# Optimization experiments

Hardware: AMD Instinct MI355X
Metric: run time of the kernel (lower is better)

Reference implementation:

```python
import jax, jax.numpy as jnp
import numpy as np

B, S, D, H = 2, 2048, 1024, 16
HD = D // H  # head dim = 64

def setup_inputs() -> dict:
    key = jax.random.key(0)
    k1, k2, k3 = jax.random.split(key, 3)
    return {
        "hidden_state": jax.random.normal(k1, (B, S, D), dtype=jnp.float32),
        "attention_mask": jnp.ones((B, S), dtype=jnp.float32),
        "w_attn": jax.random.normal(k2, (D, 3 * D), dtype=jnp.float32) * 0.02,
        "b_attn": jnp.zeros((3 * D,), dtype=jnp.float32),
        "w_proj": jax.random.normal(k3, (D, D), dtype=jnp.float32) * 0.02,
        "b_proj": jnp.zeros((D,), dtype=jnp.float32),
    }

def reference(hidden_state, attention_mask, w_attn, b_attn, w_proj, b_proj):
    x = hidden_state  # [B,S,D]
    # Conv1D: F.linear(x, weight.T, bias) == x @ weight + bias
    qkv = x @ w_attn + b_attn  # [B,S,3D]
    q, k, v = jnp.split(qkv, 3, axis=-1)
    def heads(t):  # [B,S,D] -> [B,H,S,HD]
        return t.reshape(B, S, H, HD).transpose(0, 2, 1, 3)
    q, k, v = heads(q), heads(k), heads(v)
    # scaled scores
    scores = jnp.einsum("bhqd,bhkd->bhqk", q, k) / jnp.sqrt(jnp.float32(HD))
    # mask: expand (B,S)->(B,S,S) along keys, tril, 1-that, !=0 -> -inf
    m = jnp.broadcast_to(attention_mask[:, None, :], (B, S, S))
    neg = 1.0 - jnp.tril(m)  # nonzero where disallowed
    bias = jnp.where(neg != 0.0, -jnp.inf, 0.0)  # [B,S,S]
    scores = scores + bias[:, None, :, :]
    attn = jax.nn.softmax(scores, axis=-1)  # [B,H,S,S] (dropout p=0)
    ctx = jnp.einsum("bhqk,bhkd->bhqd", attn, v)  # [B,H,S,HD]
    ctx = ctx.transpose(0, 2, 1, 3).reshape(B, S, D)
    out = ctx @ w_proj + b_proj  # resid dropout p=0
    # original returns attention.transpose(0,1): (H,B,S,S)->(B,H,S,S)
    return out, attn
```

## Files before the change

### kernel.cpp

```cpp
#include <hip/hip_runtime.h>

#define S_ 2048
#define D_ 1024
#define H_ 16
#define HD_ 64

typedef __attribute__((ext_vector_type(8))) short short8;
typedef __attribute__((ext_vector_type(4))) float floatx4;

#define MFMA16(a, b, c) __builtin_amdgcn_mfma_f32_16x16x32_bf16(a, b, c, 0, 0, 0)
#define EXP2 __builtin_amdgcn_exp2f

__device__ __forceinline__ unsigned short f2bf(float f) {
    union { float f; unsigned int u; } v; v.f = f;
    unsigned int r = v.u + 0x7FFFu + ((v.u >> 16) & 1u);
    return (unsigned short)(r >> 16);
}

__device__ __forceinline__ void gll16(const unsigned short* g, unsigned short* l) {
    __builtin_amdgcn_global_load_lds(
        (const __attribute__((address_space(1))) void*)g,
        (__attribute__((address_space(3))) void*)l, 16, 0, 0);
}

__global__ __launch_bounds__(256) void cast_bf16(const float* __restrict__ in,
                                                 unsigned short* __restrict__ out, int n4) {
    int i = blockIdx.x * 256 + threadIdx.x;
    if (i < n4) {
        float4 v = ((const float4*)in)[i];
        ushort4 o;
        o.x = f2bf(v.x); o.y = f2bf(v.y); o.z = f2bf(v.z); o.w = f2bf(v.w);
        ((ushort4*)out)[i] = o;
    }
}

__global__ __launch_bounds__(256) void transpose_cast(const float* __restrict__ W,
                                                      unsigned short* __restrict__ WT,
                                                      int K, int N) {
    __shared__ float tb[64][65];
    const int t = threadIdx.x;
    const int tr = t >> 4, tc = t & 15;
    const int n0 = blockIdx.x * 64, k0 = blockIdx.y * 64;
#pragma unroll
    for (int p = 0; p < 4; ++p) {
        const int r = p * 16 + tr;
        const float4 v = *(const float4*)&W[(size_t)(k0 + r) * N + n0 + tc * 4];
        tb[r][tc * 4 + 0] = v.x; tb[r][tc * 4 + 1] = v.y;
        tb[r][tc * 4 + 2] = v.z; tb[r][tc * 4 + 3] = v.w;
    }
    __syncthreads();
#pragma unroll
    for (int p = 0; p < 4; ++p) {
        const int rn = p * 16 + tr;
        ushort4 o;
        o.x = f2bf(tb[tc * 4 + 0][rn]); o.y = f2bf(tb[tc * 4 + 1][rn]);
        o.z = f2bf(tb[tc * 4 + 2][rn]); o.w = f2bf(tb[tc * 4 + 3][rn]);
        *(ushort4*)&WT[(size_t)(n0 + rn) * K + k0 + tc * 4] = o;
    }
}

__global__ __launch_bounds__(256) void gemm_bt(
    const unsigned short* __restrict__ A, const unsigned short* __restrict__ Bt,
    const float* __restrict__ bias, float* __restrict__ outp,
    unsigned short* __restrict__ qw, unsigned short* __restrict__ kw,
    unsigned short* __restrict__ vtw, int M, int N, int K, int mode)
{
    __shared__ unsigned short As[2][128 * 32];
    __shared__ unsigned short Bs[2][128 * 32];

    const int tid = threadIdx.x;
    const int w = tid >> 6, lane = tid & 63;
    const int l15 = lane & 15, qd = lane >> 4;
    const int wr = w >> 1, wc = w & 1;
    const int row0 = blockIdx.y * 128, col0 = blockIdx.x * 128;

    floatx4 acc[4][4];
#pragma unroll
    for (int i = 0; i < 4; ++i)
#pragma unroll
        for (int j = 0; j < 4; ++j) acc[i][j] = (floatx4){0.f, 0.f, 0.f, 0.f};

    const int sr = tid >> 2;
    const int gs = (tid & 3) ^ ((tid >> 3) & 3);
    const unsigned short* Ab0 = A + (size_t)(row0 + sr) * K + gs * 8;
    const unsigned short* Ab1 = A + (size_t)(row0 + 64 + sr) * K + gs * 8;
    const unsigned short* Bb0 = Bt + (size_t)(col0 + sr) * K + gs * 8;
    const unsigned short* Bb1 = Bt + (size_t)(col0 + 64 + sr) * K + gs * 8;

    auto stage = [&](int bi, int k0) {
        gll16(Ab0 + k0, &As[bi][tid * 8]);
        gll16(Ab1 + k0, &As[bi][(256 + tid) * 8]);
        gll16(Bb0 + k0, &Bs[bi][tid * 8]);
        gll16(Bb1 + k0, &Bs[bi][(256 + tid) * 8]);
    };

    stage(0, 0);
    const int nk = K >> 5;
    for (int it = 0; it < nk; ++it) {
        __syncthreads();
        if (it + 1 < nk) stage((it + 1) & 1, (it + 1) << 5);
        const unsigned short* Asb = As[it & 1];
        const unsigned short* Bsb = Bs[it & 1];
        short8 af[4], bfr[4];
#pragma unroll
        for (int mi = 0; mi < 4; ++mi) {
            const int ra = wr * 64 + mi * 16 + l15;
            af[mi] = *(const short8*)&Asb[ra * 32 + ((qd ^ ((ra >> 1) & 3)) << 3)];
        }
#pragma unroll
        for (int ni = 0; ni < 4; ++ni) {
            const int rb = wc * 64 + ni * 16 + l15;
            bfr[ni] = *(const short8*)&Bsb[rb * 32 + ((qd ^ ((rb >> 1) & 3)) << 3)];
        }
#pragma unroll
        for (int mi = 0; mi < 4; ++mi)
#pragma unroll
            for (int ni = 0; ni < 4; ++ni)
                acc[mi][ni] = MFMA16(af[mi], bfr[ni], acc[mi][ni]);
    }

#pragma unroll
    for (int mi = 0; mi < 4; ++mi)
#pragma unroll
        for (int ni = 0; ni < 4; ++ni) {
            const int col = col0 + wc * 64 + ni * 16 + l15;
            const float bv = bias[col];
#pragma unroll
            for (int r = 0; r < 4; ++r) {
                const int row = row0 + wr * 64 + mi * 16 + qd * 4 + r;
                const float v = acc[mi][ni][r] + bv;
                if (mode == 0) {
                    __builtin_nontemporal_store(v, &outp[(size_t)row * N + col]);
                } else {
                    const int region = col >> 10;
                    const int hh = (col >> 6) & 15;
                    const int dd = col & 63;
                    const int bb = row >> 11;
                    const int ss = row & 2047;
                    const unsigned short bvv = f2bf(v);
                    if (region == 0)
                        qw[((size_t)(bb * 16 + hh) * 2048 + ss) * 64 + dd] = bvv;
                    else if (region == 1)
                        kw[((size_t)(bb * 16 + hh) * 2048 + ss) * 64 + dd] = bvv;
                    else
                        vtw[((size_t)(bb * 16 + hh) * 64 + dd) * 2048 + ss] = bvv;
                }
            }
        }
}

__global__ __launch_bounds__(256) void attn_mfma(
    const unsigned short* __restrict__ qg, const unsigned short* __restrict__ kg,
    const unsigned short* __restrict__ vtg, const float* __restrict__ mask,
    float* __restrict__ attnOut, unsigned short* __restrict__ ctxOut)
{
    __shared__ unsigned short Qb[64 * 64];
    __shared__ unsigned short Kb[2][64 * 64];
    __shared__ unsigned short Vb[2][64 * 64];
    __shared__ unsigned short Ps[64 * 80];
    __shared__ float maskS[2][64];

    const int tid = threadIdx.x;
    const int w = tid >> 6, lane = tid & 63;
    const int l15 = lane & 15, qd = lane >> 4;
    const int x = blockIdx.x;
    const int bh = x & 31;
    const int qt = 31 - (x >> 5);
    const int b = bh >> 4, h = bh & 15;
    const size_t base = (size_t)bh * (S_ * HD_);
    const float SC = 0.18033688f;

    const int sr = tid >> 3;
    const int sp = tid & 7;
    const int gsw = sp ^ (sr & 7);

    auto stageK = [&](int bi, int jt) {
        const unsigned short* gk = kg + base + (size_t)jt * 4096;
        gll16(gk + sr * 64 + gsw * 8, &Kb[bi][tid * 8]);
        gll16(gk + (sr + 32) * 64 + gsw * 8, &Kb[bi][(256 + tid) * 8]);
    };
    auto stageV = [&](int bi, int jt) {
        const unsigned short* gv = vtg + base + jt * 64;
        gll16(gv + (size_t)sr * S_ + gsw * 8, &Vb[bi][tid * 8]);
        gll16(gv + (size_t)(sr + 32) * S_ + gsw * 8, &Vb[bi][(256 + tid) * 8]);
    };

    {
        const unsigned short* gq = qg + base + (size_t)qt * 4096;
        gll16(gq + sr * 64 + gsw * 8, &Qb[tid * 8]);
        gll16(gq + (sr + 32) * 64 + gsw * 8, &Qb[(256 + tid) * 8]);
    }
    stageK(0, 0);
    if (tid < 64) maskS[0][tid] = mask[b * S_ + tid];
    __syncthreads();

    const int qr = w * 16 + l15;
    const short8 aq0 = *(const short8*)&Qb[qr * 64 + ((qd ^ (qr & 7)) << 3)];
    const short8 aq1 = *(const short8*)&Qb[qr * 64 + (((4 + qd) ^ (qr & 7)) << 3)];

    const int qrow_base = qt * 64 + w * 16 + qd * 4;
    float m_i[4], l_i[4], rl[4];
#pragma unroll
    for (int r = 0; r < 4; ++r) { m_i[r] = -3e38f; l_i[r] = 0.f; }

    for (int jt = 0; jt <= qt; ++jt) {
        const int cb = jt & 1;
        if (jt < qt) {
            stageK(cb ^ 1, jt + 1);
            if (tid < 64) maskS[cb ^ 1][tid] = mask[b * S_ + (jt + 1) * 64 + tid];
        }
        float sv[4][4];
        bool mok[4];
        __builtin_amdgcn_s_setprio(1);
#pragma unroll
        for (int ni = 0; ni < 4; ++ni) {
            const int kr = ni * 16 + l15;
            const short8 bk0 = *(const short8*)&Kb[cb][kr * 64 + ((qd ^ (kr & 7)) << 3)];
            const short8 bk1 = *(const short8*)&Kb[cb][kr * 64 + (((4 + qd) ^ (kr & 7)) << 3)];
            floatx4 s = {0.f, 0.f, 0.f, 0.f};
            s = MFMA16(aq0, bk0, s);
            s = MFMA16(aq1, bk1, s);
#pragma unroll
            for (int r = 0; r < 4; ++r) sv[ni][r] = s[r] * SC;
            mok[ni] = (maskS[cb][kr] == 1.0f);
        }
        __builtin_amdgcn_s_setprio(0);
        const bool diag = (jt == qt);
#pragma unroll
        for (int r = 0; r < 4; ++r) {
            const int qrow = qrow_base + r;
            float svr[4], tm = -3e38f;
#pragma unroll
            for (int ni = 0; ni < 4; ++ni) {
                const bool ok = mok[ni] && (!diag || (jt * 64 + ni * 16 + l15 <= qrow));
                svr[ni] = ok ? sv[ni][r] : -3e38f;
                tm = fmaxf(tm, svr[ni]);
            }
            if (tm > -1e37f) {
                const float mn = fmaxf(m_i[r], tm);
                const float sum = EXP2(svr[0] - mn) + EXP2(svr[1] - mn) +
                                  EXP2(svr[2] - mn) + EXP2(svr[3] - mn);
                l_i[r] = l_i[r] * EXP2(m_i[r] - mn) + sum;
                m_i[r] = mn;
            }
        }
        __syncthreads();
    }

#pragma unroll
    for (int r = 0; r < 4; ++r) {
        float m = m_i[r], l = l_i[r];
#pragma unroll
        for (int off = 1; off < 16; off <<= 1) {
            const float mo = __shfl_xor(m, off);
            const float lo = __shfl_xor(l, off);
            const float mn = fmaxf(m, mo);
            l = l * EXP2(m - mn) + lo * EXP2(mo - mn);
            m = mn;
        }
        m_i[r] = m;
        rl[r] = 1.0f / l;
    }

    stageK(0, 0);
    stageV(0, 0);
    if (tid < 64) maskS[0][tid] = mask[b * S_ + tid];

    floatx4 ctxa[4];
#pragma unroll
    for (int ni = 0; ni < 4; ++ni) ctxa[ni] = (floatx4){0.f, 0.f, 0.f, 0.f};
    float* attnBH = attnOut + (size_t)bh * S_ * S_;

    for (int jt = 0; jt < 32; ++jt) {
        if (jt <= qt) {
            const int cb = jt & 1;
            __syncthreads();
            if (jt < qt) {
                stageK(cb ^ 1, jt + 1);
                stageV(cb ^ 1, jt + 1);
                if (tid < 64) maskS[cb ^ 1][tid] = mask[b * S_ + (jt + 1) * 64 + tid];
            }
            float pm[4][4];
            bool mok[4];
            __builtin_amdgcn_s_setprio(1);
#pragma unroll
            for (int ni = 0; ni < 4; ++ni) {
                const int kr = ni * 16 + l15;
                const short8 bk0 = *(const short8*)&Kb[cb][kr * 64 + ((qd ^ (kr & 7)) << 3)];
                const short8 bk1 = *(const short8*)&Kb[cb][kr * 64 + (((4 + qd) ^ (kr & 7)) << 3)];
                floatx4 s = {0.f, 0.f, 0.f, 0.f};
                s = MFMA16(aq0, bk0, s);
                s = MFMA16(aq1, bk1, s);
#pragma unroll
                for (int r = 0; r < 4; ++r) pm[ni][r] = s[r] * SC;
                mok[ni] = (maskS[cb][kr] == 1.0f);
            }
            __builtin_amdgcn_s_setprio(0);
            const bool diag = (jt == qt);
#pragma unroll
            for (int ni = 0; ni < 4; ++ni)
#pragma unroll
                for (int r = 0; r < 4; ++r) {
                    const int qrow = qrow_base + r;
                    const bool ok = mok[ni] && (!diag || (jt * 64 + ni * 16 + l15 <= qrow));
                    const float p = ok ? EXP2(pm[ni][r] - m_i[r]) * rl[r] : 0.0f;
                    pm[ni][r] = p;
                    Ps[(w * 16 + qd * 4 + r) * 80 + ni * 16 + l15] = f2bf(p);
                }
            __syncthreads();
#pragma unroll
            for (int ni = 0; ni < 4; ++ni)
#pragma unroll
                for (int r = 0; r < 4; ++r)
                    __builtin_nontemporal_store(
                        pm[ni][r],
                        &attnBH[(size_t)(qrow_base + r) * S_ + jt * 64 + ni * 16 + l15]);
            __builtin_amdgcn_s_setprio(1);
#pragma unroll
            for (int kk = 0; kk < 2; ++kk) {
                const short8 ap = *(const short8*)&Ps[(w * 16 + l15) * 80 + kk * 32 + qd * 8];
#pragma unroll
                for (int ni = 0; ni < 4; ++ni) {
                    const int vr = ni * 16 + l15;
                    const short8 bv = *(const short8*)
                        &Vb[cb][vr * 64 + (((kk * 4 + qd) ^ (vr & 7)) << 3)];
                    ctxa[ni] = MFMA16(ap, bv, ctxa[ni]);
                }
            }
            __builtin_amdgcn_s_setprio(0);
        } else {
            const floatx4 z = {0.f, 0.f, 0.f, 0.f};
#pragma unroll
            for (int p = 0; p < 4; ++p) {
                const int c = p * 256 + tid;
                const int row = c >> 4, part = c & 15;
                __builtin_nontemporal_store(
                    z, (floatx4*)&attnBH[(size_t)(qt * 64 + row) * S_ + jt * 64 + part * 4]);
            }
        }
    }

#pragma unroll
    for (int ni = 0; ni < 4; ++ni)
#pragma unroll
        for (int r = 0; r < 4; ++r) {
            const int qrow = qrow_base + r;
            ctxOut[((size_t)(b * S_ + qrow)) * D_ + h * 64 + ni * 16 + l15] =
                f2bf(ctxa[ni][r]);
        }
}

extern "C" void kernel_launch(void* const* d_in, const int* in_sizes, int n_in,
                              void* d_out, int out_size, void* d_ws, size_t ws_size,
                              hipStream_t stream) {
    const float* hidden = (const float*)d_in[0];
    const float* mask   = (const float*)d_in[1];
    const float* w_attn = (const float*)d_in[2];
    const float* b_attn = (const float*)d_in[3];
    const float* w_proj = (const float*)d_in[4];
    const float* b_proj = (const float*)d_in[5];

    float* out = (float*)d_out;
    float* attnOut = out + (size_t)2 * S_ * D_;

    unsigned short* ws = (unsigned short*)d_ws;
    const size_t E = (size_t)2 * S_ * D_;
    unsigned short* Xb   = ws;
    unsigned short* WaT  = Xb + E;
    unsigned short* WpT  = WaT + (size_t)3 * D_ * D_;
    unsigned short* qw   = WpT + (size_t)D_ * D_;
    unsigned short* kw   = qw + E;
    unsigned short* vtw  = kw + E;
    unsigned short* ctxb = vtw + E;

    dim3 blk(256);
    cast_bf16<<<dim3((int)(E / 4 / 256)), blk, 0, stream>>>(hidden, Xb, (int)(E / 4));
    transpose_cast<<<dim3(3 * D_ / 64, D_ / 64), blk, 0, stream>>>(w_attn, WaT, D_, 3 * D_);
    transpose_cast<<<dim3(D_ / 64, D_ / 64), blk, 0, stream>>>(w_proj, WpT, D_, D_);

    gemm_bt<<<dim3(3 * D_ / 128, 2 * S_ / 128), blk, 0, stream>>>(
        Xb, WaT, b_attn, nullptr, qw, kw, vtw, 2 * S_, 3 * D_, D_, 1);

    attn_mfma<<<dim3(2 * H_ * (S_ / 64)), blk, 0, stream>>>(
        qw, kw, vtw, mask, attnOut, ctxb);

    gemm_bt<<<dim3(D_ / 128, 2 * S_ / 128), blk, 0, stream>>>(
        ctxb, WpT, b_proj, out, nullptr, nullptr, nullptr, 2 * S_, D_, D_, 0);
}
```

Before: 740.3 us.

## Load K/V/Q directly from global memory and drop block-level LDS staging and barriers

Removes the double-buffered LDS staging of Q, K, V and mask, so each wave reads its MFMA operands straight from global memory (relying on L1/L2 caching) and the P tile goes into a per-wave LDS slice. This eliminates all __syncthreads barriers and lets waves run independently. In exchange, every wave re-reads the same K/V tiles from global memory with uncoalesced 16-byte per-lane loads, and no prefetching overlaps load latency. The Ps write followed by the read within a wave has no explicit wave barrier and relies on wave-synchronous execution.

After: 811.6 us. 1.1x slower.

```diff
diff --git a/kernel.cpp b/kernel.cpp
--- a/kernel.cpp
+++ b/kernel.cpp
@@ -154,11 +154,7 @@
     const unsigned short* __restrict__ vtg, const float* __restrict__ mask,
     float* __restrict__ attnOut, unsigned short* __restrict__ ctxOut)
 {
-    __shared__ unsigned short Qb[64 * 64];
-    __shared__ unsigned short Kb[2][64 * 64];
-    __shared__ unsigned short Vb[2][64 * 64];
-    __shared__ unsigned short Ps[64 * 80];
-    __shared__ float maskS[2][64];
+    __shared__ unsigned short Ps[4][16 * 80];
 
     const int tid = threadIdx.x;
     const int w = tid >> 6, lane = tid & 63;
@@ -170,33 +166,14 @@
     const size_t base = (size_t)bh * (S_ * HD_);
     const float SC = 0.18033688f;
 
-    const int sr = tid >> 3;
-    const int sp = tid & 7;
-    const int gsw = sp ^ (sr & 7);
-
-    auto stageK = [&](int bi, int jt) {
-        const unsigned short* gk = kg + base + (size_t)jt * 4096;
-        gll16(gk + sr * 64 + gsw * 8, &Kb[bi][tid * 8]);
-        gll16(gk + (sr + 32) * 64 + gsw * 8, &Kb[bi][(256 + tid) * 8]);
-    };
-    auto stageV = [&](int bi, int jt) {
-        const unsigned short* gv = vtg + base + jt * 64;
-        gll16(gv + (size_t)sr * S_ + gsw * 8, &Vb[bi][tid * 8]);
-        gll16(gv + (size_t)(sr + 32) * S_ + gsw * 8, &Vb[bi][(256 + tid) * 8]);
-    };
-
-    {
-        const unsigned short* gq = qg + base + (size_t)qt * 4096;
-        gll16(gq + sr * 64 + gsw * 8, &Qb[tid * 8]);
-        gll16(gq + (sr + 32) * 64 + gsw * 8, &Qb[(256 + tid) * 8]);
-    }
-    stageK(0, 0);
-    if (tid < 64) maskS[0][tid] = mask[b * S_ + tid];
-    __syncthreads();
-
-    const int qr = w * 16 + l15;
-    const short8 aq0 = *(const short8*)&Qb[qr * 64 + ((qd ^ (qr & 7)) << 3)];
-    const short8 aq1 = *(const short8*)&Qb[qr * 64 + (((4 + qd) ^ (qr & 7)) << 3)];
+    const unsigned short* Kbh = kg + base;
+    const unsigned short* Vbh = vtg + base;
+    const float* maskB = mask + b * S_;
+    unsigned short* Psw = &Ps[w][0];
+
+    const int qr = qt * 64 + w * 16 + l15;
+    const short8 aq0 = *(const short8*)&qg[base + (size_t)qr * 64 + qd * 8];
+    const short8 aq1 = *(const short8*)&qg[base + (size_t)qr * 64 + 32 + qd * 8];
 
     const int qrow_base = qt * 64 + w * 16 + qd * 4;
     float m_i[4], l_i[4], rl[4];
@@ -204,25 +181,21 @@
     for (int r = 0; r < 4; ++r) { m_i[r] = -3e38f; l_i[r] = 0.f; }
 
     for (int jt = 0; jt <= qt; ++jt) {
-        const int cb = jt & 1;
-        if (jt < qt) {
-            stageK(cb ^ 1, jt + 1);
-            if (tid < 64) maskS[cb ^ 1][tid] = mask[b * S_ + (jt + 1) * 64 + tid];
-        }
+        const unsigned short* Kt = Kbh + (size_t)jt * (64 * HD_);
         float sv[4][4];
         bool mok[4];
         __builtin_amdgcn_s_setprio(1);
 #pragma unroll
         for (int ni = 0; ni < 4; ++ni) {
             const int kr = ni * 16 + l15;
-            const short8 bk0 = *(const short8*)&Kb[cb][kr * 64 + ((qd ^ (kr & 7)) << 3)];
-            const short8 bk1 = *(const short8*)&Kb[cb][kr * 64 + (((4 + qd) ^ (kr & 7)) << 3)];
+            const short8 bk0 = *(const short8*)&Kt[kr * 64 + qd * 8];
+            const short8 bk1 = *(const short8*)&Kt[kr * 64 + 32 + qd * 8];
             floatx4 s = {0.f, 0.f, 0.f, 0.f};
             s = MFMA16(aq0, bk0, s);
             s = MFMA16(aq1, bk1, s);
 #pragma unroll
             for (int r = 0; r < 4; ++r) sv[ni][r] = s[r] * SC;
-            mok[ni] = (maskS[cb][kr] == 1.0f);
+            mok[ni] = (maskB[jt * 64 + kr] == 1.0f);
         }
         __builtin_amdgcn_s_setprio(0);
         const bool diag = (jt == qt);
@@ -244,7 +217,6 @@
                 m_i[r] = mn;
             }
         }
-        __syncthreads();
     }
 
 #pragma unroll
@@ -262,10 +234,6 @@
         rl[r] = 1.0f / l;
     }
 
-    stageK(0, 0);
-    stageV(0, 0);
-    if (tid < 64) maskS[0][tid] = mask[b * S_ + tid];
-
     floatx4 ctxa[4];
 #pragma unroll
     for (int ni = 0; ni < 4; ++ni) ctxa[ni] = (floatx4){0.f, 0.f, 0.f, 0.f};
@@ -273,27 +241,21 @@
 
     for (int jt = 0; jt < 32; ++jt) {
         if (jt <= qt) {
-            const int cb = jt & 1;
-            __syncthreads();
-            if (jt < qt) {
-                stageK(cb ^ 1, jt + 1);
-                stageV(cb ^ 1, jt + 1);
-                if (tid < 64) maskS[cb ^ 1][tid] = mask[b * S_ + (jt + 1) * 64 + tid];
-            }
+            const unsigned short* Kt = Kbh + (size_t)jt * (64 * HD_);
             float pm[4][4];
             bool mok[4];
             __builtin_amdgcn_s_setprio(1);
 #pragma unroll
             for (int ni = 0; ni < 4; ++ni) {
                 const int kr = ni * 16 + l15;
-                const short8 bk0 = *(const short8*)&Kb[cb][kr * 64 + ((qd ^ (kr & 7)) << 3)];
-                const short8 bk1 = *(const short8*)&Kb[cb][kr * 64 + (((4 + qd) ^ (kr & 7)) << 3)];
+                const short8 bk0 = *(const short8*)&Kt[kr * 64 + qd * 8];
+                const short8 bk1 = *(const short8*)&Kt[kr * 64 + 32 + qd * 8];
                 floatx4 s = {0.f, 0.f, 0.f, 0.f};
                 s = MFMA16(aq0, bk0, s);
                 s = MFMA16(aq1, bk1, s);
 #pragma unroll
                 for (int r = 0; r < 4; ++r) pm[ni][r] = s[r] * SC;
-                mok[ni] = (maskS[cb][kr] == 1.0f);
+                mok[ni] = (maskB[jt * 64 + kr] == 1.0f);
             }
             __builtin_amdgcn_s_setprio(0);
             const bool diag = (jt == qt);
@@ -304,26 +266,18 @@
                     const int qrow = qrow_base + r;
                     const bool ok = mok[ni] && (!diag || (jt * 64 + ni * 16 + l15 <= qrow));
                     const float p = ok ? EXP2(pm[ni][r] - m_i[r]) * rl[r] : 0.0f;
-                    pm[ni][r] = p;
-                    Ps[(w * 16 + qd * 4 + r) * 80 + ni * 16 + l15] = f2bf(p);
+                    Psw[(qd * 4 + r) * 80 + ni * 16 + l15] = f2bf(p);
+                    __builtin_nontemporal_store(
+                        p, &attnBH[(size_t)qrow * S_ + jt * 64 + ni * 16 + l15]);
                 }
-            __syncthreads();
-#pragma unroll
-            for (int ni = 0; ni < 4; ++ni)
-#pragma unroll
-                for (int r = 0; r < 4; ++r)
-                    __builtin_nontemporal_store(
-                        pm[ni][r],
-                        &attnBH[(size_t)(qrow_base + r) * S_ + jt * 64 + ni * 16 + l15]);
             __builtin_amdgcn_s_setprio(1);
 #pragma unroll
             for (int kk = 0; kk < 2; ++kk) {
-                const short8 ap = *(const short8*)&Ps[(w * 16 + l15) * 80 + kk * 32 + qd * 8];
+                const short8 ap = *(const short8*)&Psw[l15 * 80 + kk * 32 + qd * 8];
 #pragma unroll
                 for (int ni = 0; ni < 4; ++ni) {
-                    const int vr = ni * 16 + l15;
                     const short8 bv = *(const short8*)
-                        &Vb[cb][vr * 64 + (((kk * 4 + qd) ^ (vr & 7)) << 3)];
+                        &Vbh[(size_t)(ni * 16 + l15) * S_ + jt * 64 + kk * 32 + qd * 8];
                     ctxa[ni] = MFMA16(ap, bv, ctxa[ni]);
                 }
             }
```
